# Optimization experiments

Hardware: AMD Instinct MI355X
Metric: run time of the kernel (lower is better)

The kernel has to match this reference:

```python
import jax, jax.numpy as jnp
import numpy as np

B = 8
D_IN = 1024
DIM = 256
H = 8
HD = DIM // H
SIZES = [32768, 8192, 2048]
NUM_LEVELS = 3


def setup_inputs() -> dict:
    key = jax.random.key(0)
    ks = jax.random.split(key, 12)
    def p(k, shape, scale=0.02):
        return jax.random.normal(k, shape, dtype=jnp.float32) * scale
    return {
        "x": jax.random.normal(ks[0], (B, D_IN), dtype=jnp.float32),
        "proj_w": p(ks[1], (NUM_LEVELS, DIM, D_IN)),
        "proj_b": p(ks[2], (NUM_LEVELS, DIM)),
        "mem0": p(ks[3], (SIZES[0], DIM), 0.05),
        "mem1": p(ks[4], (SIZES[1], DIM), 0.05),
        "mem2": p(ks[5], (SIZES[2], DIM), 0.05),
        "inw": p(ks[6], (NUM_LEVELS, 3 * DIM, DIM)),
        "inb": p(ks[7], (NUM_LEVELS, 3 * DIM)),
        "outw": p(ks[8], (NUM_LEVELS, DIM, DIM)),
        "outb": p(ks[9], (NUM_LEVELS, DIM)),
        "merg_w": p(ks[10], (D_IN, NUM_LEVELS * DIM)),
        "merg_b": p(ks[11], (D_IN,)),
    }


def _forward(x, proj_w, proj_b, mems, inw, inb, outw, outb, merg_w, merg_b):
    level_outputs = []
    updated_memories = []
    scale = 1.0 / np.sqrt(HD).astype(np.float32)
    for i in range(NUM_LEVELS):
        # per-level projection of x: [B, DIM]
        p = x @ proj_w[i].T + proj_b[i]
        mem = mems[i]  # [S, DIM] (shared across batch, prev_memories=None path)
        wq, wk, wv = inw[i][:DIM], inw[i][DIM:2 * DIM], inw[i][2 * DIM:]
        bq, bk, bv = inb[i][:DIM], inb[i][DIM:2 * DIM], inb[i][2 * DIM:]
        q = (p @ wq.T + bq).reshape(B, H, HD)            # [B, H, HD]
        k = (mem @ wk.T + bk).reshape(-1, H, HD)         # [S, H, HD]
        v = (mem @ wv.T + bv).reshape(-1, H, HD)         # [S, H, HD]
        # single-query attention over the memory bank
        scores = jnp.einsum("bhd,shd->bhs", q, k) * scale   # [B, H, S]
        attn = jax.nn.softmax(scores, axis=-1)
        o = jnp.einsum("bhs,shd->bhd", attn, v).reshape(B, DIM)
        o = o @ outw[i].T + outb[i]                      # attention out_proj
        level_outputs.append(o)
        # broadcast memory update: [B, S, DIM]
        updated_memories.append(mem[None, :, :] + p[:, None, :])
    combined = jnp.concatenate(level_outputs, axis=-1)  # [B, 3*DIM]
    out = combined @ merg_w.T + merg_b                   # [B, D_IN]
    return (out, updated_memories[0], updated_memories[1], updated_memories[2])


def reference(x, proj_w, proj_b, mem0, mem1, mem2, inw, inb, outw, outb, merg_w, merg_b):
    return _forward(x, proj_w, proj_b, (mem0, mem1, mem2), inw, inb, outw, outb, merg_w, merg_b)
```

## Files before the change

### kernel.cpp

```cpp
#include <hip/hip_runtime.h>
#include <math.h>

#define BATCH 8
#define SCALE 0.17677669529663687f

#define WS_P    0
#define WS_QT   6144
#define WS_QBK  55296
#define WS_NUM  55488
#define WS_DEN  104640
#define WS_LVL  104832
#define WS_END  110976

#define UM0_F4 2048u
#define UM1_F4 16779264u
#define UM2_F4 20973568u

typedef float f4 __attribute__((ext_vector_type(4)));

__global__ __launch_bounds__(1024) void kA(const float* __restrict__ x,
                                           const float* __restrict__ proj_w,
                                           const float* __restrict__ proj_b,
                                           const float* __restrict__ inw,
                                           const float* __restrict__ inb,
                                           float* __restrict__ ws) {
    const int i = blockIdx.x, b = blockIdx.y, t = threadIdx.x;
    __shared__ __align__(16) float xs[1024];
    __shared__ __align__(16) float ps[256];
    __shared__ __align__(16) float qs[256];
    const int o = t >> 2, part = t & 3;

    xs[t] = x[b * 1024 + t];
    __syncthreads();

    {
        const f4* w4 = reinterpret_cast<const f4*>(proj_w + (size_t)i * 262144 + (size_t)o * 1024) + part * 64;
        const f4* x4 = reinterpret_cast<const f4*>(xs) + part * 64;
        float acc = 0.f;
        #pragma unroll 8
        for (int c = 0; c < 64; ++c) {
            f4 w = w4[c], xv = x4[c];
            acc += w.x * xv.x + w.y * xv.y + w.z * xv.z + w.w * xv.w;
        }
        acc += __shfl_xor(acc, 1);
        acc += __shfl_xor(acc, 2);
        if (part == 0) {
            const float p = acc + proj_b[i * 256 + o];
            ps[o] = p;
            ws[WS_P + i * 2048 + b * 256 + o] = p;
        }
    }
    __syncthreads();

    {
        const f4* w4 = reinterpret_cast<const f4*>(inw + (size_t)i * 196608 + (size_t)o * 256) + part * 16;
        const f4* p4 = reinterpret_cast<const f4*>(ps) + part * 16;
        float acc = 0.f;
        #pragma unroll
        for (int c = 0; c < 16; ++c) {
            f4 w = w4[c], pv = p4[c];
            acc += w.x * pv.x + w.y * pv.y + w.z * pv.z + w.w * pv.w;
        }
        acc += __shfl_xor(acc, 1);
        acc += __shfl_xor(acc, 2);
        if (part == 0) qs[o] = acc + inb[i * 768 + o];
    }
    __syncthreads();

    #pragma unroll
    for (int rep = 0; rep < 2; ++rep) {
        const int idx = rep * 1024 + t;
        const int h = idx >> 8, c = idx & 255;
        const float* wk = inw + (size_t)i * 196608 + (size_t)(256 + h * 32) * 256 + c;
        float acc = 0.f;
        #pragma unroll
        for (int d = 0; d < 32; ++d) acc += qs[h * 32 + d] * wk[(size_t)d * 256];
        ws[WS_QT + i * 16384 + (b * 8 + h) * 256 + c] = acc * SCALE;
    }
    if (t < 8) {
        float acc = 0.f;
        #pragma unroll
        for (int d = 0; d < 32; ++d) acc += qs[t * 32 + d] * inb[i * 768 + 256 + t * 32 + d];
        ws[WS_QBK + i * 64 + b * 8 + t] = acc * SCALE;
    }
}

__global__ __launch_bounds__(512) void kF(const float* __restrict__ m0,
                                          const float* __restrict__ m1,
                                          const float* __restrict__ m2,
                                          float* __restrict__ ws,
                                          float* __restrict__ out) {
    const int bx = blockIdx.x;
    const int t = threadIdx.x;
    __shared__ __align__(16) f4 lds[2][1024];

    if (bx & 1) {
        const int aid = bx >> 1;
        int lvl, s0;
        const float* mem;
        if (aid < 512)      { lvl = 0; s0 = aid << 6;         mem = m0; }
        else if (aid < 640) { lvl = 1; s0 = (aid - 512) << 6; mem = m1; }
        else                { lvl = 2; s0 = (aid - 640) << 6; mem = m2; }

        const int part = t & 15;
        const int grp = t >> 4;

        f4 qt[2][4];
        const f4* qtb = reinterpret_cast<const f4*>(ws + WS_QT + (size_t)lvl * 16384);
        #pragma unroll
        for (int bl = 0; bl < 2; ++bl)
            #pragma unroll
            for (int g = 0; g < 4; ++g)
                qt[bl][g] = qtb[(size_t)(grp * 2 + bl) * 64 + part + 16 * g];
        float qbk[2];
        #pragma unroll
        for (int bl = 0; bl < 2; ++bl) qbk[bl] = ws[WS_QBK + lvl * 64 + grp * 2 + bl];

        f4 nr[2][4];
        #pragma unroll
        for (int bl = 0; bl < 2; ++bl)
            #pragma unroll
            for (int g = 0; g < 4; ++g) nr[bl][g] = 0.f;
        float dn0 = 0.f, dn1 = 0.f;

        const f4* gm = reinterpret_cast<const f4*>(mem) + (size_t)s0 * 64;
        f4 st[2];
        #pragma unroll
        for (int k = 0; k < 2; ++k) st[k] = gm[t + 512 * k];
        #pragma unroll
        for (int k = 0; k < 2; ++k) lds[0][t + 512 * k] = st[k];
        __syncthreads();

        for (int tile = 0; tile < 4; ++tile) {
            if (tile < 3) {
                #pragma unroll
                for (int k = 0; k < 2; ++k) st[k] = gm[(size_t)(tile + 1) * 1024 + t + 512 * k];
            }
            const f4* buf = lds[tile & 1];
            for (int r = 0; r < 16; ++r) {
                f4 m4[4];
                #pragma unroll
                for (int g = 0; g < 4; ++g) m4[g] = buf[r * 64 + part + 16 * g];
                float sc0 = 0.f, sc1 = 0.f;
                #pragma unroll
                for (int g = 0; g < 4; ++g) {
                    sc0 += qt[0][g].x * m4[g].x + qt[0][g].y * m4[g].y + qt[0][g].z * m4[g].z + qt[0][g].w * m4[g].w;
                    sc1 += qt[1][g].x * m4[g].x + qt[1][g].y * m4[g].y + qt[1][g].z * m4[g].z + qt[1][g].w * m4[g].w;
                }
                sc0 += __shfl_xor(sc0, 1); sc1 += __shfl_xor(sc1, 1);
                sc0 += __shfl_xor(sc0, 2); sc1 += __shfl_xor(sc1, 2);
                sc0 += __shfl_xor(sc0, 4); sc1 += __shfl_xor(sc1, 4);
                sc0 += __shfl_xor(sc0, 8); sc1 += __shfl_xor(sc1, 8);
                const float e0 = __expf(sc0 + qbk[0]);
                const float e1 = __expf(sc1 + qbk[1]);
                dn0 += e0; dn1 += e1;
                #pragma unroll
                for (int g = 0; g < 4; ++g) { nr[0][g] += e0 * m4[g]; nr[1][g] += e1 * m4[g]; }
            }
            if (tile < 3) {
                #pragma unroll
                for (int k = 0; k < 2; ++k) lds[(tile + 1) & 1][t + 512 * k] = st[k];
                __syncthreads();
            }
        }

        #pragma unroll
        for (int bl = 0; bl < 2; ++bl) {
            const int bh = grp * 2 + bl;
            float* np = ws + WS_NUM + (size_t)lvl * 16384 + bh * 256 + part * 4;
            #pragma unroll
            for (int g = 0; g < 4; ++g) {
                #pragma unroll
                for (int j = 0; j < 4; ++j) atomicAdd(np + 64 * g + j, nr[bl][g][j]);
            }
            if (part == 0) atomicAdd(ws + WS_DEN + lvl * 64 + bh, bl == 0 ? dn0 : dn1);
        }
    } else {
        const int wid = bx >> 1;
        int lvl, b;
        size_t mbase4, obase4;
        const float* mem;
        if (wid < 512) {
            lvl = 0; b = wid >> 6; const int ch = wid & 63; mem = m0;
            mbase4 = (size_t)ch << 15;
            obase4 = UM0_F4 + ((size_t)b << 21) + ((size_t)ch << 15);
        } else if (wid < 640) {
            const int w = wid - 512; lvl = 1; b = w >> 4; const int ch = w & 15; mem = m1;
            mbase4 = (size_t)ch << 15;
            obase4 = UM1_F4 + ((size_t)b << 19) + ((size_t)ch << 15);
        } else {
            const int w = wid - 640; lvl = 2; b = w >> 2; const int ch = w & 3; mem = m2;
            mbase4 = (size_t)ch << 15;
            obase4 = UM2_F4 + ((size_t)b << 17) + ((size_t)ch << 15);
        }
        const f4 pr = reinterpret_cast<const f4*>(ws + WS_P + (size_t)lvl * 2048 + b * 256)[t & 63];

        const f4* src = reinterpret_cast<const f4*>(mem) + mbase4;
        f4* dst = reinterpret_cast<f4*>(out) + obase4;
        for (int it = 0; it < 64; it += 8) {
            f4 v[8];
            #pragma unroll
            for (int j = 0; j < 8; ++j) v[j] = src[((size_t)(it + j) << 9) + t];
            #pragma unroll
            for (int j = 0; j < 8; ++j) dst[((size_t)(it + j) << 9) + t] = v[j] + pr;
        }
    }
}

__global__ __launch_bounds__(1024) void kC(const float* __restrict__ inw,
                                           const float* __restrict__ inb,
                                           const float* __restrict__ outw,
                                           const float* __restrict__ outb,
                                           float* __restrict__ ws) {
    const int i = blockIdx.x, b = blockIdx.y, t = threadIdx.x;
    __shared__ __align__(16) float a[2048];
    __shared__ __align__(16) float ao[256];

    #pragma unroll
    for (int rep = 0; rep < 2; ++rep) {
        const int idx = rep * 1024 + t;
        a[idx] = ws[WS_NUM + i * 16384 + b * 2048 + idx] / ws[WS_DEN + i * 64 + b * 8 + (idx >> 8)];
    }
    __syncthreads();

    const int o = t >> 2, part = t & 3;
    {
        const f4* w4 = reinterpret_cast<const f4*>(inw + (size_t)i * 196608 + (size_t)(512 + o) * 256) + part * 16;
        const f4* a4 = reinterpret_cast<const f4*>(a + (o >> 5) * 256) + part * 16;
        float acc = 0.f;
        #pragma unroll
        for (int c = 0; c < 16; ++c) {
            f4 w = w4[c], av = a4[c];
            acc += w.x * av.x + w.y * av.y + w.z * av.z + w.w * av.w;
        }
        acc += __shfl_xor(acc, 1);
        acc += __shfl_xor(acc, 2);
        if (part == 0) ao[o] = acc + inb[i * 768 + 512 + o];
    }
    __syncthreads();
    {
        const f4* w4 = reinterpret_cast<const f4*>(outw + (size_t)i * 65536 + (size_t)o * 256) + part * 16;
        const f4* a4 = reinterpret_cast<const f4*>(ao) + part * 16;
        float acc = 0.f;
        #pragma unroll
        for (int c = 0; c < 16; ++c) {
            f4 w = w4[c], av = a4[c];
            acc += w.x * av.x + w.y * av.y + w.z * av.z + w.w * av.w;
        }
        acc += __shfl_xor(acc, 1);
        acc += __shfl_xor(acc, 2);
        if (part == 0) ws[WS_LVL + i * 2048 + b * 256 + o] = acc + outb[i * 256 + o];
    }
}

__global__ __launch_bounds__(1024) void kD(const float* __restrict__ merg_w,
                                           const float* __restrict__ merg_b,
                                           const float* __restrict__ ws,
                                           float* __restrict__ out) {
    const int b = blockIdx.x, quarter = blockIdx.y, t = threadIdx.x;
    __shared__ __align__(16) float comb[768];
    if (t < 768) comb[t] = ws[WS_LVL + (t >> 8) * 2048 + b * 256 + (t & 255)];
    __syncthreads();

    const int j = quarter * 256 + (t >> 2), part = t & 3;
    const f4* w4 = reinterpret_cast<const f4*>(merg_w + (size_t)j * 768) + part * 48;
    const f4* c4 = reinterpret_cast<const f4*>(comb) + part * 48;
    float acc = 0.f;
    #pragma unroll 8
    for (int c = 0; c < 48; ++c) {
        f4 w = w4[c], cv = c4[c];
        acc += w.x * cv.x + w.y * cv.y + w.z * cv.z + w.w * cv.w;
    }
    acc += __shfl_xor(acc, 1);
    acc += __shfl_xor(acc, 2);
    if (part == 0) out[b * 1024 + j] = acc + merg_b[j];
}

extern "C" void kernel_launch(void* const* d_in, const int* in_sizes, int n_in,
                              void* d_out, int out_size, void* d_ws, size_t ws_size,
                              hipStream_t stream) {
    const float* x      = (const float*)d_in[0];
    const float* proj_w = (const float*)d_in[1];
    const float* proj_b = (const float*)d_in[2];
    const float* mem0   = (const float*)d_in[3];
    const float* mem1   = (const float*)d_in[4];
    const float* mem2   = (const float*)d_in[5];
    const float* inw    = (const float*)d_in[6];
    const float* inb    = (const float*)d_in[7];
    const float* outw   = (const float*)d_in[8];
    const float* outb   = (const float*)d_in[9];
    const float* mw     = (const float*)d_in[10];
    const float* mb     = (const float*)d_in[11];
    float* out = (float*)d_out;
    float* ws  = (float*)d_ws;

    hipMemsetAsync(ws + WS_NUM, 0, (size_t)(WS_LVL - WS_NUM) * sizeof(float), stream);

    kA<<<dim3(3, 8), 1024, 0, stream>>>(x, proj_w, proj_b, inw, inb, ws);
    kF<<<1344, 512, 0, stream>>>(mem0, mem1, mem2, ws, out);
    kC<<<dim3(3, 8), 1024, 0, stream>>>(inw, inb, outw, outb, ws);
    kD<<<dim3(8, 4), 1024, 0, stream>>>(mw, mb, ws, out);
}
```

Baseline: 359.0 us.

## Read each memory row once for all batches and fold workspace zeroing into kA

The broadcast-update blocks now load each 16-row memory tile once and write it out for all 8 batch entries with the matching projection added. Before, each block handled one batch's slice, so the memory bank was re-read 8 times. The grid is re-interleaved as 4 update blocks per attention block. The separate hipMemsetAsync is dropped, and kA zeroes the atomic accumulation area instead, saving a launch. The risks are scattered write strides across batches and the kA zeroing racing with later use, although stream order protects it.

```diff
diff --git a/kernel.cpp b/kernel.cpp
--- a/kernel.cpp
+++ b/kernel.cpp
@@ -11,6 +11,7 @@
 #define WS_DEN  104640
 #define WS_LVL  104832
 #define WS_END  110976
+#define WS_ZN   (WS_DEN + 192 - WS_NUM)
 
 #define UM0_F4 2048u
 #define UM1_F4 16779264u
@@ -30,6 +31,16 @@
     __shared__ __align__(16) float qs[256];
     const int o = t >> 2, part = t & 3;
 
+    {
+        const int bid = i * 8 + b;
+        const int base = bid * 2056;
+        #pragma unroll
+        for (int rep = 0; rep < 3; ++rep) {
+            const int k = base + rep * 1024 + t;
+            if (k < base + 2056 && k < WS_ZN) ws[WS_NUM + k] = 0.f;
+        }
+    }
+
     xs[t] = x[b * 1024 + t];
     __syncthreads();
 
@@ -94,8 +105,8 @@
     const int t = threadIdx.x;
     __shared__ __align__(16) f4 lds[2][1024];
 
-    if (bx & 1) {
-        const int aid = bx >> 1;
+    if (bx % 5 == 4) {
+        const int aid = bx / 5;
         int lvl, s0;
         const float* mem;
         if (aid < 512)      { lvl = 0; s0 = aid << 6;         mem = m0; }
@@ -176,33 +187,34 @@
             if (part == 0) atomicAdd(ws + WS_DEN + lvl * 64 + bh, bl == 0 ? dn0 : dn1);
         }
     } else {
-        const int wid = bx >> 1;
-        int lvl, b;
-        size_t mbase4, obase4;
+        const int wid = (bx / 5) * 4 + (bx % 5);
+        int lvl, logS;
+        size_t row0, ob4;
         const float* mem;
-        if (wid < 512) {
-            lvl = 0; b = wid >> 6; const int ch = wid & 63; mem = m0;
-            mbase4 = (size_t)ch << 15;
-            obase4 = UM0_F4 + ((size_t)b << 21) + ((size_t)ch << 15);
-        } else if (wid < 640) {
-            const int w = wid - 512; lvl = 1; b = w >> 4; const int ch = w & 15; mem = m1;
-            mbase4 = (size_t)ch << 15;
-            obase4 = UM1_F4 + ((size_t)b << 19) + ((size_t)ch << 15);
-        } else {
-            const int w = wid - 640; lvl = 2; b = w >> 2; const int ch = w & 3; mem = m2;
-            mbase4 = (size_t)ch << 15;
-            obase4 = UM2_F4 + ((size_t)b << 17) + ((size_t)ch << 15);
-        }
-        const f4 pr = reinterpret_cast<const f4*>(ws + WS_P + (size_t)lvl * 2048 + b * 256)[t & 63];
-
-        const f4* src = reinterpret_cast<const f4*>(mem) + mbase4;
-        f4* dst = reinterpret_cast<f4*>(out) + obase4;
-        for (int it = 0; it < 64; it += 8) {
-            f4 v[8];
+        if (wid < 2048)      { lvl = 0; row0 = (size_t)wid << 4;          ob4 = UM0_F4; logS = 15; mem = m0; }
+        else if (wid < 2560) { lvl = 1; row0 = (size_t)(wid - 2048) << 4; ob4 = UM1_F4; logS = 13; mem = m1; }
+        else                 { lvl = 2; row0 = (size_t)(wid - 2560) << 4; ob4 = UM2_F4; logS = 11; mem = m2; }
+
+        const int r = t >> 6;
+        const int c4 = t & 63;
+        f4 pr[8];
+        #pragma unroll
+        for (int b = 0; b < 8; ++b)
+            pr[b] = reinterpret_cast<const f4*>(ws + WS_P + (size_t)lvl * 2048 + b * 256)[c4];
+
+        const f4* mem4 = reinterpret_cast<const f4*>(mem);
+        f4* o4 = reinterpret_cast<f4*>(out) + ob4;
+
+        f4 mv[2];
+        #pragma unroll
+        for (int k = 0; k < 2; ++k)
+            mv[k] = mem4[(row0 + k * 8 + r) * 64 + c4];
+        #pragma unroll
+        for (int k = 0; k < 2; ++k) {
+            const size_t row = row0 + k * 8 + r;
             #pragma unroll
-            for (int j = 0; j < 8; ++j) v[j] = src[((size_t)(it + j) << 9) + t];
-            #pragma unroll
-            for (int j = 0; j < 8; ++j) dst[((size_t)(it + j) << 9) + t] = v[j] + pr;
+            for (int b = 0; b < 8; ++b)
+                o4[((size_t)(b << logS) + row) * 64 + c4] = mv[k] + pr[b];
         }
     }
 }
@@ -294,10 +306,8 @@
     float* out = (float*)d_out;
     float* ws  = (float*)d_ws;
 
-    hipMemsetAsync(ws + WS_NUM, 0, (size_t)(WS_LVL - WS_NUM) * sizeof(float), stream);
-
     kA<<<dim3(3, 8), 1024, 0, stream>>>(x, proj_w, proj_b, inw, inb, ws);
-    kF<<<1344, 512, 0, stream>>>(mem0, mem1, mem2, ws, out);
+    kF<<<3360, 512, 0, stream>>>(mem0, mem1, mem2, ws, out);
     kC<<<dim3(3, 8), 1024, 0, stream>>>(inw, inb, outw, outb, ws);
     kD<<<dim3(8, 4), 1024, 0, stream>>>(mw, mb, ws, out);
 }
```

New measurement: 342.0 us. 4.7% less time.
